# Kernel tuning notes

Measured on AMD Instinct MI355X. Metric: run time of the kernel, lower is better.

The kernel has to match this reference:

```python
import jax, jax.numpy as jnp
import numpy as np

N_NODES = 50000
IN_DIM = 128
HID = 2 * IN_DIM  # 256, per module: hidden_dim = input_dims * 2
FC1 = 1024
FC2 = 512
N_ACT = 64
N_EDGES = 800000
N_AGENTS = 16384


def _layernorm(h, g, b, eps=1e-5):
    mu = jnp.mean(h, axis=-1, keepdims=True)
    var = jnp.var(h, axis=-1, keepdims=True)
    return (h - mu) * jax.lax.rsqrt(var + eps) * g + b


def setup_inputs() -> dict:
    key = jax.random.key(0)
    ks = jax.random.split(key, 16)
    def u(k, shape, fan_in):
        s = 1.0 / np.sqrt(fan_in)
        return jax.random.uniform(k, shape, jnp.float32, -s, s)
    inp = {}
    inp["x"] = jax.random.normal(ks[0], (N_NODES, IN_DIM), jnp.float32)
    inp["action"] = jax.random.normal(ks[1], (N_AGENTS, N_ACT), jnp.float32)
    inp["edge_index"] = jax.random.randint(ks[2], (2, N_EDGES), 0, N_NODES, jnp.int32)
    inp["agent_idx"] = jax.random.randint(ks[3], (N_AGENTS,), 0, N_NODES, jnp.int32)
    # GCNConv params (linear no bias + separate bias)
    inp["W_gcn"] = u(ks[4], (IN_DIM, HID), IN_DIM)
    inp["b_gcn"] = jnp.zeros((HID,), jnp.float32)
    # fc1, fc2 (custom uniform init per module)
    inp["W1"] = u(ks[5], (HID, FC1), FC1)
    inp["b1"] = u(ks[6], (FC1,), FC1)
    inp["g1"] = jnp.ones((FC1,), jnp.float32)
    inp["beta1"] = jnp.zeros((FC1,), jnp.float32)
    inp["W2"] = u(ks[7], (FC1, FC2), FC2)
    inp["b2"] = u(ks[8], (FC2,), FC2)
    inp["g2"] = jnp.ones((FC2,), jnp.float32)
    inp["beta2"] = jnp.zeros((FC2,), jnp.float32)
    inp["Wa"] = u(ks[9], (N_ACT, FC2), FC2)
    inp["ba"] = u(ks[10], (FC2,), FC2)
    inp["Wq"] = jax.random.uniform(ks[11], (FC2, 1), jnp.float32, -0.003, 0.003)
    inp["bq"] = jax.random.uniform(ks[12], (1,), jnp.float32, -0.003, 0.003)
    return inp


def reference(x, action, W_gcn, b_gcn, W1, b1, g1, beta1, W2, b2, g2, beta2, Wa, ba, Wq, bq, edge_index, agent_idx):
    N = x.shape[0]
    # GCNConv: add self-loops, symmetric D^-1/2 (A+I) D^-1/2 normalization
    loops = jnp.arange(N, dtype=edge_index.dtype)
    src = jnp.concatenate([edge_index[0], loops])
    dst = jnp.concatenate([edge_index[1], loops])
    h = x @ W_gcn  # [N, HID] transform before aggregation
    deg = jax.ops.segment_sum(jnp.ones_like(dst, dtype=h.dtype), dst, num_segments=N)
    dinv = jax.lax.rsqrt(jnp.maximum(deg, 1.0))  # deg >= 1 due to self-loops
    norm = dinv[src] * dinv[dst]  # [E+N]
    agg = jax.ops.segment_sum(h[src] * norm[:, None], dst, num_segments=N) + b_gcn
    # masked gather of agent nodes, then critic MLP
    z = jax.nn.relu(agg[agent_idx])  # [A, HID]
    s = jax.nn.relu(_layernorm(z @ W1 + b1, g1, beta1))
    s = _layernorm(s @ W2 + b2, g2, beta2)
    a = action @ Wa + ba
    sa = jax.nn.relu(s + a)
    return sa @ Wq + bq  # [A, 1]
```

## Files before the change

kernel.cpp:

```cpp
#include <hip/hip_runtime.h>
#include <hip/hip_bf16.h>

typedef _Float16 f16;
typedef _Float16 __attribute__((ext_vector_type(8))) half8;
typedef _Float16 __attribute__((ext_vector_type(4))) half4;
typedef float __attribute__((ext_vector_type(4))) floatx4;

#define IN_DIM 128
#define HID    256
#define FC1    1024
#define FC2    512
#define NACT   64
#define BUCKET 128

__device__ __forceinline__ void transpose_tile(const float* __restrict__ in, f16* __restrict__ out,
                                               int K, int N, int bx, int by, int tid) {
    __shared__ f16 tile[32][33];
    int k0 = bx * 32, n0 = by * 32;
    int tx = tid & 31, ty = tid >> 5;
    #pragma unroll
    for (int i = 0; i < 4; ++i)
        tile[ty + i * 8][tx] = (f16)in[(size_t)(k0 + ty + i * 8) * N + n0 + tx];
    __syncthreads();
    #pragma unroll
    for (int i = 0; i < 4; ++i)
        out[(size_t)(n0 + ty + i * 8) * K + k0 + tx] = tile[tx][ty + i * 8];
}

__device__ __forceinline__ void cvt8(const float* __restrict__ in, f16* __restrict__ out, long gi) {
    float4 a = *(const float4*)&in[gi * 8];
    float4 b = *(const float4*)&in[gi * 8 + 4];
    half8 pk;
    pk[0] = (f16)a.x; pk[1] = (f16)a.y; pk[2] = (f16)a.z; pk[3] = (f16)a.w;
    pk[4] = (f16)b.x; pk[5] = (f16)b.y; pk[6] = (f16)b.z; pk[7] = (f16)b.w;
    *(half8*)&out[gi * 8] = pk;
}

__global__ __launch_bounds__(256)
void prep_kernel(const float* __restrict__ Wgcn, const float* __restrict__ W1,
                 const float* __restrict__ W2, const float* __restrict__ Wa,
                 const float* __restrict__ action, const float* __restrict__ x,
                 f16* WgcnT, f16* W1T, f16* W2T, f16* WaT, f16* act16, f16* x16,
                 int* degcnt, int* needed, int* n_needed, int* cursor, int N, int A) {
    int b = blockIdx.x, tid = threadIdx.x;
    if (b < 196) {
        int i = b * 256 + tid;
        if (i < N) { degcnt[i] = 0; needed[i] = 0; }
        if (b == 0 && tid == 0) *n_needed = 0;
        return;
    }
    b -= 196;
    if (b < 64)  { cursor[b * 256 + tid] = 0; return; }
    b -= 64;
    if (b < 32)  { transpose_tile(Wgcn, WgcnT, IN_DIM, HID, b & 3, b >> 2, tid); return; }
    b -= 32;
    if (b < 256) { transpose_tile(W1, W1T, HID, FC1, b & 7, b >> 3, tid); return; }
    b -= 256;
    if (b < 512) { transpose_tile(W2, W2T, FC1, FC2, b & 31, b >> 5, tid); return; }
    b -= 512;
    if (b < 32)  { transpose_tile(Wa, WaT, NACT, FC2, b & 1, b >> 1, tid); return; }
    b -= 32;
    if (b < 512) { cvt8(action, act16, (long)b * 256 + tid); return; }
    b -= 512;
    cvt8(x, x16, (long)b * 256 + tid);
}

__global__ void markdeg_kernel(const int* __restrict__ agent_idx, const int* __restrict__ edst,
                               int* __restrict__ needed, int* __restrict__ needed_list,
                               int* __restrict__ n_needed, int* __restrict__ degcnt, int A, int E) {
    int b = blockIdx.x;
    if (b < 64) {
        int i = b * 256 + threadIdx.x;
        if (i < A) {
            int idx = agent_idx[i];
            if (atomicCAS(&needed[idx], 0, -1) == 0) {
                int p = atomicAdd(n_needed, 1);
                needed_list[p] = idx;
                needed[idx] = p + 1;
            }
        }
        return;
    }
    int e = (b - 64) * 256 + threadIdx.x;
    if (e < E) atomicAdd(&degcnt[edst[e]], 1);
}

__global__ void fill_kernel(const int* __restrict__ esrc, const int* __restrict__ edst,
                            const int* __restrict__ needed, int* __restrict__ cursor,
                            int* __restrict__ srcbuf, int E) {
    int e = blockIdx.x * 256 + threadIdx.x;
    if (e < E) {
        int d = edst[e];
        int s = needed[d];
        if (s != 0) {
            int slot = s - 1;
            int pos = atomicAdd(&cursor[slot], 1);
            if (pos < BUCKET) srcbuf[(size_t)slot * BUCKET + pos] = esrc[e];
        }
    }
}

__global__ __launch_bounds__(256)
void gather_x_kernel(const int* __restrict__ needed_list, const int* __restrict__ n_needed,
                     const int* __restrict__ degcnt, const int* __restrict__ srcbuf,
                     const f16* __restrict__ x16, f16* __restrict__ xagg) {
    int w = (blockIdx.x * 256 + threadIdx.x) >> 6;
    int lane = threadIdx.x & 63;
    if (w >= *n_needed) return;
    int d = needed_list[w];
    float dd = rsqrtf((float)degcnt[d] + 1.0f);
    size_t beg = (size_t)w * BUCKET;
    int cnt = degcnt[d];
    if (cnt > BUCKET) cnt = BUCKET;
    union { unsigned u; f16 h[2]; } ld0, ld1, ld2, ld3;
    ld0.u = *(const unsigned*)&x16[(size_t)d * IN_DIM + lane * 2];
    float ax = (float)ld0.h[0] * dd * dd, ay = (float)ld0.h[1] * dd * dd;
    int j = 0;
    for (; j + 3 < cnt; j += 4) {
        int s0 = srcbuf[beg + j], s1 = srcbuf[beg + j + 1];
        int s2 = srcbuf[beg + j + 2], s3 = srcbuf[beg + j + 3];
        float n0 = rsqrtf((float)degcnt[s0] + 1.0f) * dd;
        float n1 = rsqrtf((float)degcnt[s1] + 1.0f) * dd;
        float n2 = rsqrtf((float)degcnt[s2] + 1.0f) * dd;
        float n3 = rsqrtf((float)degcnt[s3] + 1.0f) * dd;
        ld0.u = *(const unsigned*)&x16[(size_t)s0 * IN_DIM + lane * 2];
        ld1.u = *(const unsigned*)&x16[(size_t)s1 * IN_DIM + lane * 2];
        ld2.u = *(const unsigned*)&x16[(size_t)s2 * IN_DIM + lane * 2];
        ld3.u = *(const unsigned*)&x16[(size_t)s3 * IN_DIM + lane * 2];
        ax = fmaf((float)ld0.h[0], n0, ax); ay = fmaf((float)ld0.h[1], n0, ay);
        ax = fmaf((float)ld1.h[0], n1, ax); ay = fmaf((float)ld1.h[1], n1, ay);
        ax = fmaf((float)ld2.h[0], n2, ax); ay = fmaf((float)ld2.h[1], n2, ay);
        ax = fmaf((float)ld3.h[0], n3, ax); ay = fmaf((float)ld3.h[1], n3, ay);
    }
    for (; j < cnt; ++j) {
        int s0 = srcbuf[beg + j];
        float n0 = rsqrtf((float)degcnt[s0] + 1.0f) * dd;
        ld0.u = *(const unsigned*)&x16[(size_t)s0 * IN_DIM + lane * 2];
        ax = fmaf((float)ld0.h[0], n0, ax);
        ay = fmaf((float)ld0.h[1], n0, ay);
    }
    union { f16 h[2]; unsigned u; } pk;
    pk.h[0] = (f16)ax; pk.h[1] = (f16)ay;
    *(unsigned*)&xagg[(size_t)w * IN_DIM + lane * 2] = pk.u;
}

__device__ __forceinline__ void swz_decode(int bid, int log2ny, int& bx, int& by) {
    int xcd = bid & 7;
    int pos = bid >> 3;
    bx = (pos >> log2ny) * 8 + xcd;
    by = pos & ((1 << log2ny) - 1);
}

template<bool RELU, bool LIMIT>
__device__ __forceinline__ void gemm_tile64(f16* __restrict__ smA, f16* __restrict__ smB,
                                            const f16* __restrict__ A, const f16* __restrict__ BT,
                                            f16* __restrict__ C, const float* __restrict__ bias,
                                            const int* __restrict__ limit,
                                            int bx, int by, int N, int K) {
    if (LIMIT && bx * 64 >= *limit) return;
    const int tid = threadIdx.x;
    const int lane = tid & 63;
    const int wave = tid >> 6;
    const int wr = wave >> 1, wc = wave & 1;
    const long bm = (long)bx * 64, bn = (long)by * 64;

    size_t aoff[2], boff[2];
    #pragma unroll
    for (int t = 0; t < 2; ++t) {
        int ci = t * 256 + tid;
        int r = ci >> 3, s = ci & 7, ks = s ^ (r & 7);
        aoff[t] = (size_t)(bm + r) * K + ks * 8;
        boff[t] = (size_t)(bn + r) * K + ks * 8;
    }
    int aidx[2][2], bidx[2][2];
    const int kc = lane >> 4;
    #pragma unroll
    for (int kk = 0; kk < 2; ++kk) {
        #pragma unroll
        for (int i = 0; i < 2; ++i) {
            int ar = wr * 32 + i * 16 + (lane & 15);
            aidx[kk][i] = ar * 64 + ((kk * 4 + kc) ^ (ar & 7)) * 8;
            int br = wc * 32 + i * 16 + (lane & 15);
            bidx[kk][i] = br * 64 + ((kk * 4 + kc) ^ (br & 7)) * 8;
        }
    }

    const int NT = K >> 6;
    auto stage = [&](int buf, int k0) {
        #pragma unroll
        for (int t = 0; t < 2; ++t) {
            __builtin_amdgcn_global_load_lds(
                (const __attribute__((address_space(1))) void*)(A + aoff[t] + k0),
                (__attribute__((address_space(3))) void*)(&smA[buf * 4096 + (t * 256 + tid) * 8]), 16, 0, 0);
            __builtin_amdgcn_global_load_lds(
                (const __attribute__((address_space(1))) void*)(BT + boff[t] + k0),
                (__attribute__((address_space(3))) void*)(&smB[buf * 4096 + (t * 256 + tid) * 8]), 16, 0, 0);
        }
    };

    floatx4 acc[2][2] = {};
    stage(0, 0);
    asm volatile("s_waitcnt vmcnt(0)" ::: "memory");
    __builtin_amdgcn_s_barrier();
    int cur = 0;
    for (int t = 0; t < NT; ++t) {
        if (t + 1 < NT) stage(cur ^ 1, (t + 1) << 6);
        #pragma unroll
        for (int kk = 0; kk < 2; ++kk) {
            half8 af[2], bf[2];
            #pragma unroll
            for (int i = 0; i < 2; ++i) {
                af[i] = *(const half8*)&smA[cur * 4096 + aidx[kk][i]];
                bf[i] = *(const half8*)&smB[cur * 4096 + bidx[kk][i]];
            }
            #pragma unroll
            for (int mi = 0; mi < 2; ++mi)
                #pragma unroll
                for (int ni = 0; ni < 2; ++ni)
                    acc[mi][ni] = __builtin_amdgcn_mfma_f32_16x16x32_f16(af[mi], bf[ni], acc[mi][ni], 0, 0, 0);
        }
        asm volatile("s_waitcnt vmcnt(0)" ::: "memory");
        __builtin_amdgcn_s_barrier();
        cur ^= 1;
    }
    const int col0 = (int)bn + wc * 32 + (lane & 15);
    const int row0 = (int)bm + wr * 32 + (lane >> 4) * 4;
    #pragma unroll
    for (int ni = 0; ni < 2; ++ni) {
        int col = col0 + ni * 16;
        float bz = bias[col];
        #pragma unroll
        for (int mi = 0; mi < 2; ++mi) {
            #pragma unroll
            for (int q = 0; q < 4; ++q) {
                int row = row0 + mi * 16 + q;
                float v = acc[mi][ni][q] + bz;
                if (RELU) v = fmaxf(v, 0.f);
                C[(size_t)row * N + col] = (f16)v;
            }
        }
    }
}

template<bool RELU, bool LIMIT>
__global__ __launch_bounds__(256)
void gemm64_kernel(const f16* __restrict__ A, const f16* __restrict__ BT,
                   f16* __restrict__ C, const float* __restrict__ bias,
                   const int* __restrict__ limit, int N, int K, int log2ny) {
    __shared__ __align__(16) f16 smA[2 * 4096];
    __shared__ __align__(16) f16 smB[2 * 4096];
    int bx, by;
    swz_decode(blockIdx.x, log2ny, bx, by);
    gemm_tile64<RELU, LIMIT>(smA, smB, A, BT, C, bias, limit, bx, by, N, K);
}

template<bool LIMIT>
__device__ __forceinline__ void gemm_tile128(f16* __restrict__ smA, f16* __restrict__ smB,
                                             const f16* __restrict__ A, const f16* __restrict__ BT,
                                             f16* __restrict__ C, const float* __restrict__ bias,
                                             const int* __restrict__ limit,
                                             int bx, int by, int N, int K) {
    if (LIMIT && bx * 128 >= *limit) return;
    const int tid = threadIdx.x;
    const int lane = tid & 63;
    const int wave = tid >> 6;
    const int wr = wave >> 1, wc = wave & 1;
    const long bm = (long)bx * 128, bn = (long)by * 128;

    size_t aoff[4], boff[4];
    #pragma unroll
    for (int t = 0; t < 4; ++t) {
        int ci = t * 256 + tid;
        int r = ci >> 3, s = ci & 7, ks = s ^ (r & 7);
        aoff[t] = (size_t)(bm + r) * K + ks * 8;
        boff[t] = (size_t)(bn + r) * K + ks * 8;
    }
    int aidx[2][4], bidx[2][4];
    const int kc = lane >> 4;
    #pragma unroll
    for (int kk = 0; kk < 2; ++kk) {
        #pragma unroll
        for (int i = 0; i < 4; ++i) {
            int ar = wr * 64 + i * 16 + (lane & 15);
            aidx[kk][i] = ar * 64 + ((kk * 4 + kc) ^ (ar & 7)) * 8;
            int br = wc * 64 + i * 16 + (lane & 15);
            bidx[kk][i] = br * 64 + ((kk * 4 + kc) ^ (br & 7)) * 8;
        }
    }

    const int NT = K >> 6;
    auto stage = [&](int buf, int k0) {
        #pragma unroll
        for (int t = 0; t < 4; ++t) {
            __builtin_amdgcn_global_load_lds(
                (const __attribute__((address_space(1))) void*)(A + aoff[t] + k0),
                (__attribute__((address_space(3))) void*)(&smA[buf * 8192 + (t * 256 + tid) * 8]), 16, 0, 0);
            __builtin_amdgcn_global_load_lds(
                (const __attribute__((address_space(1))) void*)(BT + boff[t] + k0),
                (__attribute__((address_space(3))) void*)(&smB[buf * 8192 + (t * 256 + tid) * 8]), 16, 0, 0);
        }
    };

    floatx4 acc[4][4] = {};
    stage(0, 0);
    asm volatile("s_waitcnt vmcnt(0)" ::: "memory");
    __builtin_amdgcn_s_barrier();
    int cur = 0;
    for (int t = 0; t < NT; ++t) {
        if (t + 1 < NT) stage(cur ^ 1, (t + 1) << 6);
        #pragma unroll
        for (int kk = 0; kk < 2; ++kk) {
            half8 af[4], bf[4];
            #pragma unroll
            for (int i = 0; i < 4; ++i) {
                af[i] = *(const half8*)&smA[cur * 8192 + aidx[kk][i]];
                bf[i] = *(const half8*)&smB[cur * 8192 + bidx[kk][i]];
            }
            #pragma unroll
            for (int mi = 0; mi < 4; ++mi)
                #pragma unroll
                for (int ni = 0; ni < 4; ++ni)
                    acc[mi][ni] = __builtin_amdgcn_mfma_f32_16x16x32_f16(af[mi], bf[ni], acc[mi][ni], 0, 0, 0);
        }
        asm volatile("s_waitcnt vmcnt(0)" ::: "memory");
        __builtin_amdgcn_s_barrier();
        cur ^= 1;
    }
    const int col0 = (int)bn + wc * 64 + (lane & 15);
    const int row0 = (int)bm + wr * 64 + (lane >> 4) * 4;
    #pragma unroll
    for (int ni = 0; ni < 4; ++ni) {
        int col = col0 + ni * 16;
        float bz = bias[col];
        #pragma unroll
        for (int mi = 0; mi < 4; ++mi) {
            #pragma unroll
            for (int q = 0; q < 4; ++q) {
                int row = row0 + mi * 16 + q;
                C[(size_t)row * N + col] = (f16)(acc[mi][ni][q] + bz);
            }
        }
    }
}

template<bool LIMIT>
__global__ __launch_bounds__(256)
void gemm128_kernel(const f16* __restrict__ A, const f16* __restrict__ BT,
                    f16* __restrict__ C, const float* __restrict__ bias,
                    const int* __restrict__ limit, int N, int K, int log2ny) {
    __shared__ __align__(16) f16 smA[2 * 8192];
    __shared__ __align__(16) f16 smB[2 * 8192];
    int bx, by;
    swz_decode(blockIdx.x, log2ny, bx, by);
    gemm_tile128<LIMIT>(smA, smB, A, BT, C, bias, limit, bx, by, N, K);
}

__global__ __launch_bounds__(256)
void gemm_dual_kernel(const f16* __restrict__ A0, const f16* __restrict__ BT0, f16* __restrict__ C0,
                      const float* __restrict__ bias0, const int* __restrict__ limit, int K0,
                      const f16* __restrict__ A1, const f16* __restrict__ BT1, f16* __restrict__ C1,
                      const float* __restrict__ bias1, int K1, int half, int N) {
    __shared__ __align__(16) f16 smA[2 * 8192];
    __shared__ __align__(16) f16 smB[2 * 8192];
    int bid = blockIdx.x;
    int bx, by;
    if (bid < half) {
        swz_decode(bid, 2, bx, by);
        gemm_tile128<true>(smA, smB, A0, BT0, C0, bias0, limit, bx, by, N, K0);
    } else {
        swz_decode(bid - half, 2, bx, by);
        gemm_tile128<false>(smA, smB, A1, BT1, C1, bias1, nullptr, bx, by, N, K1);
    }
}

__global__ __launch_bounds__(256)
void ln_relu_f16_kernel(f16* __restrict__ s, const float* __restrict__ g,
                        const float* __restrict__ b, const int* __restrict__ nn) {
    int row = blockIdx.x;
    if (row >= *nn) return;
    f16* p = s + (size_t)row * FC1;
    int tid = threadIdx.x;
    half4 v = *(const half4*)&p[tid * 4];
    float f0 = (float)v[0], f1 = (float)v[1], f2 = (float)v[2], f3 = (float)v[3];
    float sum = f0 + f1 + f2 + f3;
    float sq = f0 * f0 + f1 * f1 + f2 * f2 + f3 * f3;
    #pragma unroll
    for (int off = 32; off > 0; off >>= 1) {
        sum += __shfl_down(sum, off);
        sq  += __shfl_down(sq, off);
    }
    __shared__ float ssum[4], ssq[4];
    int wid = tid >> 6;
    if ((tid & 63) == 0) { ssum[wid] = sum; ssq[wid] = sq; }
    __syncthreads();
    float tot = ssum[0] + ssum[1] + ssum[2] + ssum[3];
    float tq  = ssq[0] + ssq[1] + ssq[2] + ssq[3];
    float mu = tot * (1.0f / FC1);
    float var = tq * (1.0f / FC1) - mu * mu;
    float rs = rsqrtf(var + 1e-5f);
    float4 gg = *(const float4*)&g[tid * 4];
    float4 bb = *(const float4*)&b[tid * 4];
    half4 o;
    o[0] = (f16)fmaxf((f0 - mu) * rs * gg.x + bb.x, 0.f);
    o[1] = (f16)fmaxf((f1 - mu) * rs * gg.y + bb.y, 0.f);
    o[2] = (f16)fmaxf((f2 - mu) * rs * gg.z + bb.z, 0.f);
    o[3] = (f16)fmaxf((f3 - mu) * rs * gg.w + bb.w, 0.f);
    *(half4*)&p[tid * 4] = o;
}

__global__ __launch_bounds__(256)
void final_f16_kernel(const f16* __restrict__ s2, const f16* __restrict__ ab,
                      const int* __restrict__ agent_idx, const int* __restrict__ needed,
                      const float* __restrict__ g2, const float* __restrict__ b2,
                      const float* __restrict__ Wq, const float* __restrict__ bq,
                      float* __restrict__ out) {
    int row = blockIdx.x;
    int slot = needed[agent_idx[row]] - 1;
    const f16* p = s2 + (size_t)slot * FC2;
    int tid = threadIdx.x;
    float v0 = (float)p[tid * 2], v1 = (float)p[tid * 2 + 1];
    float sum = v0 + v1;
    float sq = v0 * v0 + v1 * v1;
    #pragma unroll
    for (int off = 32; off > 0; off >>= 1) {
        sum += __shfl_down(sum, off);
        sq  += __shfl_down(sq, off);
    }
    __shared__ float ssum[4], ssq[4], spart[4];
    int wid = tid >> 6;
    if ((tid & 63) == 0) { ssum[wid] = sum; ssq[wid] = sq; }
    __syncthreads();
    float tot = ssum[0] + ssum[1] + ssum[2] + ssum[3];
    float tq  = ssq[0] + ssq[1] + ssq[2] + ssq[3];
    float mu = tot * (1.0f / FC2);
    float var = tq * (1.0f / FC2) - mu * mu;
    float rs = rsqrtf(var + 1e-5f);
    float a0 = (float)ab[(size_t)row * FC2 + tid * 2];
    float a1 = (float)ab[(size_t)row * FC2 + tid * 2 + 1];
    float g0 = g2[tid * 2], g1 = g2[tid * 2 + 1];
    float bb0 = b2[tid * 2], bb1 = b2[tid * 2 + 1];
    float sa0 = fmaxf((v0 - mu) * rs * g0 + bb0 + a0, 0.f);
    float sa1 = fmaxf((v1 - mu) * rs * g1 + bb1 + a1, 0.f);
    float part = sa0 * Wq[tid * 2] + sa1 * Wq[tid * 2 + 1];
    #pragma unroll
    for (int off = 32; off > 0; off >>= 1) part += __shfl_down(part, off);
    if ((tid & 63) == 0) spart[wid] = part;
    __syncthreads();
    if (tid == 0) out[row] = spart[0] + spart[1] + spart[2] + spart[3] + bq[0];
}

extern "C" void kernel_launch(void* const* d_in, const int* in_sizes, int n_in,
                              void* d_out, int out_size, void* d_ws, size_t ws_size,
                              hipStream_t stream) {
    const float* x        = (const float*)d_in[0];
    const float* action   = (const float*)d_in[1];
    const int*   edge     = (const int*)d_in[2];
    const int*   agent_idx= (const int*)d_in[3];
    const float* W_gcn    = (const float*)d_in[4];
    const float* b_gcn    = (const float*)d_in[5];
    const float* W1       = (const float*)d_in[6];
    const float* b1       = (const float*)d_in[7];
    const float* g1       = (const float*)d_in[8];
    const float* beta1    = (const float*)d_in[9];
    const float* W2       = (const float*)d_in[10];
    const float* b2       = (const float*)d_in[11];
    const float* g2       = (const float*)d_in[12];
    const float* beta2    = (const float*)d_in[13];
    const float* Wa       = (const float*)d_in[14];
    const float* ba       = (const float*)d_in[15];
    const float* Wq       = (const float*)d_in[16];
    const float* bq       = (const float*)d_in[17];
    float* out = (float*)d_out;

    const int N = in_sizes[0] / IN_DIM;
    const int E = in_sizes[2] / 2;
    const int A = in_sizes[3];
    const int* esrc = edge;
    const int* edst = edge + E;

    char* ws = (char*)d_ws;
    size_t off = 0;
    auto carve = [&](size_t bytes) -> char* {
        char* p = ws + off;
        off += (bytes + 255) & ~(size_t)255;
        return p;
    };
    int*   degcnt     = (int*)  carve((size_t)N * 4);
    int*   needed     = (int*)  carve((size_t)N * 4);
    int*   cursor     = (int*)  carve((size_t)A * 4);
    int*   needed_list= (int*)  carve((size_t)A * 4);
    int*   n_needed   = (int*)  carve(256);
    int*   srcbuf     = (int*)  carve((size_t)A * BUCKET * 4);
    f16*   WgcnT      = (f16*)  carve((size_t)HID * IN_DIM * 2);
    f16*   W1T        = (f16*)  carve((size_t)FC1 * HID * 2);
    f16*   W2T        = (f16*)  carve((size_t)FC2 * FC1 * 2);
    f16*   WaT        = (f16*)  carve((size_t)FC2 * NACT * 2);
    f16*   act16      = (f16*)  carve((size_t)A * NACT * 2);
    f16*   x16        = (f16*)  carve((size_t)N * IN_DIM * 2);
    f16*   xagg       = (f16*)  carve((size_t)A * IN_DIM * 2);
    f16*   z          = (f16*)  carve((size_t)A * HID * 2);
    f16*   s1         = (f16*)  carve((size_t)A * FC1 * 2);
    f16*   s2         = (f16*)  carve((size_t)A * FC2 * 2);
    f16*   abuf       = (f16*)  carve((size_t)A * FC2 * 2);
    (void)ws_size;

    const int eblk = (E + 255) / 256;

    prep_kernel<<<196 + 64 + 32 + 256 + 512 + 32 + 512 + eblk, 256, 0, stream>>>(
        W_gcn, W1, W2, Wa, action, x, WgcnT, W1T, W2T, WaT, act16, x16,
        degcnt, needed, n_needed, cursor, N, A);
    markdeg_kernel<<<64 + eblk, 256, 0, stream>>>(agent_idx, edst, needed, needed_list,
                                                  n_needed, degcnt, A, E);
    fill_kernel<<<eblk, 256, 0, stream>>>(esrc, edst, needed, cursor, srcbuf, E);
    gather_x_kernel<<<(A + 3) / 4, 256, 0, stream>>>(needed_list, n_needed, degcnt,
                                                     srcbuf, x16, xagg);
    gemm64_kernel<true, true><<<(A / 64) * (HID / 64), 256, 0, stream>>>(
        xagg, WgcnT, z, b_gcn, n_needed, HID, IN_DIM, 2);
    gemm128_kernel<true><<<(A / 128) * (FC1 / 128), 256, 0, stream>>>(
        z, W1T, s1, b1, n_needed, FC1, HID, 3);
    ln_relu_f16_kernel<<<A, 256, 0, stream>>>(s1, g1, beta1, n_needed);
    gemm_dual_kernel<<<2 * (A / 128) * (FC2 / 128), 256, 0, stream>>>(
        s1, W2T, s2, b2, n_needed, FC1,
        act16, WaT, abuf, ba, NACT, (A / 128) * (FC2 / 128), FC2);
    final_f16_kernel<<<A, 256, 0, stream>>>(s2, abuf, agent_idx, needed, g2, beta2, Wq, bq, out);
}
```

Before: 160.6 us.

## Gather fp32 x directly and stage GEMM epilogues through LDS for vector stores

Removes the pass that converts all of x to fp16. The gather kernel now reads fp32 rows of x directly, since only the neighbours of agent nodes are ever touched. Separately, the GEMM epilogues write each wave's output sub-tile into shared memory and then issue 16-byte row-contiguous stores instead of scattered 2-byte stores. The trade-off is twice the bytes per gathered row and extra barriers in the epilogue.

```diff
diff --git a/kernel.cpp b/kernel.cpp
--- a/kernel.cpp
+++ b/kernel.cpp
@@ -39,8 +39,8 @@
 __global__ __launch_bounds__(256)
 void prep_kernel(const float* __restrict__ Wgcn, const float* __restrict__ W1,
                  const float* __restrict__ W2, const float* __restrict__ Wa,
-                 const float* __restrict__ action, const float* __restrict__ x,
-                 f16* WgcnT, f16* W1T, f16* W2T, f16* WaT, f16* act16, f16* x16,
+                 const float* __restrict__ action,
+                 f16* WgcnT, f16* W1T, f16* W2T, f16* WaT, f16* act16,
                  int* degcnt, int* needed, int* n_needed, int* cursor, int N, int A) {
     int b = blockIdx.x, tid = threadIdx.x;
     if (b < 196) {
@@ -60,9 +60,7 @@
     b -= 512;
     if (b < 32)  { transpose_tile(Wa, WaT, NACT, FC2, b & 1, b >> 1, tid); return; }
     b -= 32;
-    if (b < 512) { cvt8(action, act16, (long)b * 256 + tid); return; }
-    b -= 512;
-    cvt8(x, x16, (long)b * 256 + tid);
+    cvt8(action, act16, (long)b * 256 + tid);
 }
 
 __global__ void markdeg_kernel(const int* __restrict__ agent_idx, const int* __restrict__ edst,
@@ -103,7 +101,7 @@
 __global__ __launch_bounds__(256)
 void gather_x_kernel(const int* __restrict__ needed_list, const int* __restrict__ n_needed,
                      const int* __restrict__ degcnt, const int* __restrict__ srcbuf,
-                     const f16* __restrict__ x16, f16* __restrict__ xagg) {
+                     const float* __restrict__ x, f16* __restrict__ xagg) {
     int w = (blockIdx.x * 256 + threadIdx.x) >> 6;
     int lane = threadIdx.x & 63;
     if (w >= *n_needed) return;
@@ -112,9 +110,8 @@
     size_t beg = (size_t)w * BUCKET;
     int cnt = degcnt[d];
     if (cnt > BUCKET) cnt = BUCKET;
-    union { unsigned u; f16 h[2]; } ld0, ld1, ld2, ld3;
-    ld0.u = *(const unsigned*)&x16[(size_t)d * IN_DIM + lane * 2];
-    float ax = (float)ld0.h[0] * dd * dd, ay = (float)ld0.h[1] * dd * dd;
+    float2 xs = *(const float2*)&x[(size_t)d * IN_DIM + lane * 2];
+    float ax = xs.x * dd * dd, ay = xs.y * dd * dd;
     int j = 0;
     for (; j + 3 < cnt; j += 4) {
         int s0 = srcbuf[beg + j], s1 = srcbuf[beg + j + 1];
@@ -123,21 +120,21 @@
         float n1 = rsqrtf((float)degcnt[s1] + 1.0f) * dd;
         float n2 = rsqrtf((float)degcnt[s2] + 1.0f) * dd;
         float n3 = rsqrtf((float)degcnt[s3] + 1.0f) * dd;
-        ld0.u = *(const unsigned*)&x16[(size_t)s0 * IN_DIM + lane * 2];
-        ld1.u = *(const unsigned*)&x16[(size_t)s1 * IN_DIM + lane * 2];
-        ld2.u = *(const unsigned*)&x16[(size_t)s2 * IN_DIM + lane * 2];
-        ld3.u = *(const unsigned*)&x16[(size_t)s3 * IN_DIM + lane * 2];
-        ax = fmaf((float)ld0.h[0], n0, ax); ay = fmaf((float)ld0.h[1], n0, ay);
-        ax = fmaf((float)ld1.h[0], n1, ax); ay = fmaf((float)ld1.h[1], n1, ay);
-        ax = fmaf((float)ld2.h[0], n2, ax); ay = fmaf((float)ld2.h[1], n2, ay);
-        ax = fmaf((float)ld3.h[0], n3, ax); ay = fmaf((float)ld3.h[1], n3, ay);
+        float2 v0 = *(const float2*)&x[(size_t)s0 * IN_DIM + lane * 2];
+        float2 v1 = *(const float2*)&x[(size_t)s1 * IN_DIM + lane * 2];
+        float2 v2 = *(const float2*)&x[(size_t)s2 * IN_DIM + lane * 2];
+        float2 v3 = *(const float2*)&x[(size_t)s3 * IN_DIM + lane * 2];
+        ax = fmaf(v0.x, n0, ax); ay = fmaf(v0.y, n0, ay);
+        ax = fmaf(v1.x, n1, ax); ay = fmaf(v1.y, n1, ay);
+        ax = fmaf(v2.x, n2, ax); ay = fmaf(v2.y, n2, ay);
+        ax = fmaf(v3.x, n3, ax); ay = fmaf(v3.y, n3, ay);
     }
     for (; j < cnt; ++j) {
         int s0 = srcbuf[beg + j];
         float n0 = rsqrtf((float)degcnt[s0] + 1.0f) * dd;
-        ld0.u = *(const unsigned*)&x16[(size_t)s0 * IN_DIM + lane * 2];
-        ax = fmaf((float)ld0.h[0], n0, ax);
-        ay = fmaf((float)ld0.h[1], n0, ay);
+        float2 v0 = *(const float2*)&x[(size_t)s0 * IN_DIM + lane * 2];
+        ax = fmaf(v0.x, n0, ax);
+        ay = fmaf(v0.y, n0, ay);
     }
     union { f16 h[2]; unsigned u; } pk;
     pk.h[0] = (f16)ax; pk.h[1] = (f16)ay;
@@ -223,22 +220,26 @@
         __builtin_amdgcn_s_barrier();
         cur ^= 1;
     }
-    const int col0 = (int)bn + wc * 32 + (lane & 15);
-    const int row0 = (int)bm + wr * 32 + (lane >> 4) * 4;
-    #pragma unroll
-    for (int ni = 0; ni < 2; ++ni) {
-        int col = col0 + ni * 16;
-        float bz = bias[col];
-        #pragma unroll
-        for (int mi = 0; mi < 2; ++mi) {
+    f16* scr = smA + wave * 512;
+    #pragma unroll
+    for (int mi = 0; mi < 2; ++mi) {
+        __syncthreads();
+        #pragma unroll
+        for (int ni = 0; ni < 2; ++ni) {
+            int c = ni * 16 + (lane & 15);
+            float bz = bias[bn + wc * 32 + c];
             #pragma unroll
             for (int q = 0; q < 4; ++q) {
-                int row = row0 + mi * 16 + q;
+                int r = (lane >> 4) * 4 + q;
                 float v = acc[mi][ni][q] + bz;
                 if (RELU) v = fmaxf(v, 0.f);
-                C[(size_t)row * N + col] = (f16)v;
+                scr[r * 32 + c] = (f16)v;
             }
         }
+        __syncthreads();
+        int r = lane >> 2, ch = lane & 3;
+        half8 v = *(const half8*)&scr[r * 32 + ch * 8];
+        *(half8*)&C[(size_t)(bm + wr * 32 + mi * 16 + r) * N + (bn + wc * 32 + ch * 8)] = v;
     }
 }
 
@@ -326,19 +327,27 @@
         __builtin_amdgcn_s_barrier();
         cur ^= 1;
     }
-    const int col0 = (int)bn + wc * 64 + (lane & 15);
-    const int row0 = (int)bm + wr * 64 + (lane >> 4) * 4;
-    #pragma unroll
-    for (int ni = 0; ni < 4; ++ni) {
-        int col = col0 + ni * 16;
-        float bz = bias[col];
-        #pragma unroll
-        for (int mi = 0; mi < 4; ++mi) {
+    f16* scr = smA + wave * 1024;
+    #pragma unroll
+    for (int mi = 0; mi < 4; ++mi) {
+        __syncthreads();
+        #pragma unroll
+        for (int ni = 0; ni < 4; ++ni) {
+            int c = ni * 16 + (lane & 15);
+            float bz = bias[bn + wc * 64 + c];
             #pragma unroll
             for (int q = 0; q < 4; ++q) {
-                int row = row0 + mi * 16 + q;
-                C[(size_t)row * N + col] = (f16)(acc[mi][ni][q] + bz);
+                int r = (lane >> 4) * 4 + q;
+                scr[r * 64 + c] = (f16)(acc[mi][ni][q] + bz);
             }
+        }
+        __syncthreads();
+        #pragma unroll
+        for (int it = 0; it < 2; ++it) {
+            int flat = it * 64 + lane;
+            int r = flat >> 3, ch = flat & 7;
+            half8 v = *(const half8*)&scr[r * 64 + ch * 8];
+            *(half8*)&C[(size_t)(bm + wr * 64 + mi * 16 + r) * N + (bn + wc * 64 + ch * 8)] = v;
         }
     }
 }
@@ -496,7 +505,6 @@
     f16*   W2T        = (f16*)  carve((size_t)FC2 * FC1 * 2);
     f16*   WaT        = (f16*)  carve((size_t)FC2 * NACT * 2);
     f16*   act16      = (f16*)  carve((size_t)A * NACT * 2);
-    f16*   x16        = (f16*)  carve((size_t)N * IN_DIM * 2);
     f16*   xagg       = (f16*)  carve((size_t)A * IN_DIM * 2);
     f16*   z          = (f16*)  carve((size_t)A * HID * 2);
     f16*   s1         = (f16*)  carve((size_t)A * FC1 * 2);
@@ -506,14 +514,14 @@
 
     const int eblk = (E + 255) / 256;
 
-    prep_kernel<<<196 + 64 + 32 + 256 + 512 + 32 + 512 + eblk, 256, 0, stream>>>(
-        W_gcn, W1, W2, Wa, action, x, WgcnT, W1T, W2T, WaT, act16, x16,
+    prep_kernel<<<196 + 64 + 32 + 256 + 512 + 32 + 512, 256, 0, stream>>>(
+        W_gcn, W1, W2, Wa, action, WgcnT, W1T, W2T, WaT, act16,
         degcnt, needed, n_needed, cursor, N, A);
     markdeg_kernel<<<64 + eblk, 256, 0, stream>>>(agent_idx, edst, needed, needed_list,
                                                   n_needed, degcnt, A, E);
     fill_kernel<<<eblk, 256, 0, stream>>>(esrc, edst, needed, cursor, srcbuf, E);
     gather_x_kernel<<<(A + 3) / 4, 256, 0, stream>>>(needed_list, n_needed, degcnt,
-                                                     srcbuf, x16, xagg);
+                                                     srcbuf, x, xagg);
     gemm64_kernel<true, true><<<(A / 64) * (HID / 64), 256, 0, stream>>>(
         xagg, WgcnT, z, b_gcn, n_needed, HID, IN_DIM, 2);
     gemm128_kernel<true><<<(A / 128) * (FC1 / 128), 256, 0, stream>>>(
```

Result: no change. 161.6 us (+0.7%).
